# Kernel optimization log

Hardware: AMD Instinct MI355X
Metric: run time of the kernel (lower is better)

## Reference

```python
import jax, jax.numpy as jnp
import numpy as np

V, D, H, B, T = 50000, 256, 512, 64, 512
FORGET_BIAS = 1.0  # TF LSTMCell default

def setup_inputs() -> dict:
    key = jax.random.key(0)
    k1, k2, k3, k4 = jax.random.split(key, 4)
    word_indices = jax.random.randint(k1, (B, T), 0, V, dtype=jnp.int32)
    num_words = jax.random.randint(k2, (B,), 1, T + 1, dtype=jnp.int32)
    # Embedding: uniform(-1, 1) per original
    W_emb = jax.random.uniform(k3, (V, D), minval=-1.0, maxval=1.0, dtype=jnp.float32)
    # TF LSTMCell: single kernel [(D+H), 4H] with gate order i, j, f, o; zero bias
    kernel = jax.random.normal(k4, (D + H, 4 * H), dtype=jnp.float32) * 0.02
    bias = jnp.zeros((4 * H,), dtype=jnp.float32)
    return {"word_indices": word_indices, "num_words": num_words,
            "W_emb": W_emb, "kernel": kernel, "bias": bias}

def reference(word_indices, num_words, W_emb, kernel, bias):
    # embedding lookup: [B, T, D]
    x = W_emb[word_indices]
    xs = jnp.swapaxes(x, 0, 1)  # [T, B, D] time-major
    ts = jnp.arange(xs.shape[0])
    c0 = jnp.zeros((word_indices.shape[0], H), dtype=x.dtype)
    h0 = jnp.zeros_like(c0)

    def step(carry, inp):
        c, h = carry
        x_t, t = inp
        gates = jnp.concatenate([x_t, h], axis=-1) @ kernel + bias  # [B, 4H]
        i, j, f, o = jnp.split(gates, 4, axis=-1)
        c_new = jax.nn.sigmoid(f + FORGET_BIAS) * c + jax.nn.sigmoid(i) * jnp.tanh(j)
        h_new = jax.nn.sigmoid(o) * jnp.tanh(c_new)
        # static_rnn sequence_length semantics: copy state through past the end
        mask = (t < num_words)[:, None]
        c = jnp.where(mask, c_new, c)
        h = jnp.where(mask, h_new, h)
        return (c, h), None

    (c_fin, h_fin), _ = jax.lax.scan(step, (c0, h0), (xs, ts))
    # TF LSTM final_state = LSTMStateTuple(c, h); stack for a single array output
    return jnp.stack([c_fin, h_fin], axis=0)  # [2, B, H]
```

## Files before the change

kernel.cpp:

```cpp
#include <hip/hip_runtime.h>
#include <stdint.h>


#define NWG     64
#define NTHR    256
#define TSTEPS  512
#define BATCH   64
#define EDIM    256
#define HID     512
#define GCOLS   2048

typedef __attribute__((ext_vector_type(8))) short short8;
typedef __attribute__((ext_vector_type(4))) float f32x4;


__device__ __forceinline__ unsigned short f2bf(float f) {
  unsigned u = __float_as_uint(f);
  unsigned r = (u + 0x7FFFu + ((u >> 16) & 1u)) >> 16;
  return (unsigned short)r;
}
__device__ __forceinline__ float sigf(float x) {
  x = fminf(fmaxf(x, -30.0f), 30.0f);
  return 1.0f / (1.0f + __expf(-x));
}
__device__ __forceinline__ float tanh_fast(float x) {
  x = fminf(fmaxf(x, -15.0f), 15.0f);
  float e = __expf(-2.0f * x);
  return (1.0f - e) / (1.0f + e);
}
__device__ __forceinline__ void lstm_cell(float gi, float gj, float gf, float go,
                                          int t, int nw, float& c, float& h) {
  float cn = sigf(gf + 1.0f) * c + sigf(gi) * tanh_fast(gj);
  float hn = sigf(go) * tanh_fast(cn);
  if (t < nw) { c = cn; h = hn; }
}

__global__ void init_ws(unsigned* ws, int nwords) {
  int i = blockIdx.x * 256 + threadIdx.x;
  if (i < nwords) ws[i] = 0u;
}

__global__ void embed_k(const int* __restrict__ widx, const float* __restrict__ Wemb,
                        unsigned short* __restrict__ xb) {
  int tb = blockIdx.x;
  int t = tb >> 6, b = tb & 63;
  int wi = widx[b * TSTEPS + t];
  const float* src = Wemb + (size_t)wi * EDIM + threadIdx.x * 4;
  float4 v = *(const float4*)src;
  ushort4 o;
  o.x = f2bf(v.x); o.y = f2bf(v.y); o.z = f2bf(v.z); o.w = f2bf(v.w);
  *(ushort4*)(xb + (size_t)tb * EDIM + threadIdx.x * 4) = o;
}

__launch_bounds__(NTHR, 1)
__global__ void lstm_persist(const int* __restrict__ num_words,
                             const int* __restrict__ widx,
                             const float* __restrict__ Wemb,
                             const float* __restrict__ Wk,
                             const float* __restrict__ bias,
                             const unsigned short* __restrict__ xb,
                             unsigned short* __restrict__ hb0,
                             unsigned short* __restrict__ hb1,
                             unsigned* flags,
                             float* __restrict__ out,
                             int has_xb)
{
  __shared__ alignas(16) short Wlds[24576];
  __shared__ alignas(16) unsigned short hstg[1024];

  const int tid  = threadIdx.x;
  const int lane = tid & 63;
  const int wv   = tid >> 6;
  const int u0   = blockIdx.x * 8;

  for (int q = tid; q < 3072; q += NTHR) {
    int lq = q & 63;
    int kkn = q >> 6;
    int nt = (kkn >= 24) ? 1 : 0;
    int kk = kkn - nt * 24;
    int kbase = kk * 32 + ((lq >> 4) << 3);
    int nn = (nt << 4) + (lq & 15);
    int gcol = ((nn >> 3) << 9) + u0 + (nn & 7);
    short8 v;
#pragma unroll
    for (int j = 0; j < 8; ++j)
      v[j] = (short)f2bf(Wk[(size_t)(kbase + j) * GCOLS + gcol]);
    *(short8*)&Wlds[q * 8] = v;
  }

  const int n   = lane & 15;
  const int q4  = lane >> 4;
  const int bb  = wv * 16 + n;
  const int kq  = q4 << 3;
  const int un  = n & 7;
  const bool lo = (n < 8);

  float bias_g[4];
#pragma unroll
  for (int g = 0; g < 4; ++g) bias_g[g] = bias[g * HID + u0 + un];
  int nw_r[4];
#pragma unroll
  for (int r = 0; r < 4; ++r) nw_r[r] = num_words[wv * 16 + q4 * 4 + r];

  float c_r[4] = {0.f, 0.f, 0.f, 0.f};
  float h_r[4] = {0.f, 0.f, 0.f, 0.f};

  unsigned* myflag = flags + ((blockIdx.x << 2) + wv) * 32;
  const unsigned* fp = flags + ((lane << 2) + wv) * 32;

  unsigned short* hb[2] = {hb0, hb1};

  float4 pfw[16];
  uint4  pfx[8];
  auto PREFETCH = [&](int tt) {
    if (has_xb) {
      const unsigned short* xrow = xb + ((size_t)tt * BATCH + bb) * EDIM + kq;
#pragma unroll
      for (int kk = 0; kk < 8; ++kk)
        pfx[kk] = *(const uint4*)(xrow + kk * 32);
    } else {
      int wi = widx[bb * TSTEPS + tt];
      const float* er = Wemb + (size_t)wi * EDIM + kq;
#pragma unroll
      for (int kk = 0; kk < 8; ++kk) {
        pfw[2 * kk]     = *(const float4*)(er + kk * 32);
        pfw[2 * kk + 1] = *(const float4*)(er + kk * 32 + 4);
      }
    }
  };
  PREFETCH(0);

  __syncthreads();

  for (int t = 0; t < TSTEPS; ++t) {
    f32x4 acc0 = {0.f, 0.f, 0.f, 0.f};
    f32x4 acc1 = {0.f, 0.f, 0.f, 0.f};
    uint4 av[16];

    if (t > 0) {
      const unsigned tgt = (unsigned)t;
      for (;;) {
        unsigned v;
        asm volatile("global_load_dword %0, %1, off sc0 sc1\n\t"
                     "s_waitcnt vmcnt(0)" : "=v"(v) : "v"(fp));
        if (__ballot(v >= tgt) == ~0ull) break;
      }
      const unsigned short* hr = hb[t & 1] + bb * HID + kq;
#pragma unroll
      for (int kk = 0; kk < 16; ++kk)
        asm volatile("global_load_dwordx4 %0, %1, off sc0 sc1"
                     : "=v"(av[kk]) : "v"(hr + kk * 32));
    }

#pragma unroll
    for (int kk = 0; kk < 8; ++kk) {
      short8 a;
      if (has_xb) {
        a = __builtin_bit_cast(short8, pfx[kk]);
      } else {
        float4 f0 = pfw[2 * kk], f1 = pfw[2 * kk + 1];
        a[0] = (short)f2bf(f0.x); a[1] = (short)f2bf(f0.y);
        a[2] = (short)f2bf(f0.z); a[3] = (short)f2bf(f0.w);
        a[4] = (short)f2bf(f1.x); a[5] = (short)f2bf(f1.y);
        a[6] = (short)f2bf(f1.z); a[7] = (short)f2bf(f1.w);
      }
      short8 w0 = *(const short8*)&Wlds[((kk)      * 64 + lane) * 8];
      short8 w1 = *(const short8*)&Wlds[((24 + kk) * 64 + lane) * 8];
      acc0 = __builtin_amdgcn_mfma_f32_16x16x32_bf16(a, w0, acc0, 0, 0, 0);
      acc1 = __builtin_amdgcn_mfma_f32_16x16x32_bf16(a, w1, acc1, 0, 0, 0);
    }

    if (t > 0) {
      asm volatile("s_waitcnt vmcnt(0)" ::: "memory");
      __builtin_amdgcn_sched_barrier(0);
#pragma unroll
      for (int kk = 0; kk < 16; ++kk) {
        short8 a  = __builtin_bit_cast(short8, av[kk]);
        short8 w0 = *(const short8*)&Wlds[((8 + kk)  * 64 + lane) * 8];
        short8 w1 = *(const short8*)&Wlds[((32 + kk) * 64 + lane) * 8];
        acc0 = __builtin_amdgcn_mfma_f32_16x16x32_bf16(a, w0, acc0, 0, 0, 0);
        acc1 = __builtin_amdgcn_mfma_f32_16x16x32_bf16(a, w1, acc1, 0, 0, 0);
      }
    }

#pragma unroll
    for (int r = 0; r < 4; ++r) {
      float a0o = acc0[r], a1o = acc1[r];
      float a0x = __shfl_xor(a0o, 8);
      float a1x = __shfl_xor(a1o, 8);
      float gi = lo ? a0o : a0x;
      float gj = lo ? a0x : a0o;
      float gf = lo ? a1o : a1x;
      float go = lo ? a1x : a1o;
      lstm_cell(gi + bias_g[0], gj + bias_g[1], gf + bias_g[2], go + bias_g[3],
                t, nw_r[r], c_r[r], h_r[r]);
    }

    if (t + 1 < TSTEPS) {
      unsigned short* hw = hb[(t + 1) & 1];
      if (lo) {
#pragma unroll
        for (int r = 0; r < 4; ++r)
          hstg[wv * 256 + (q4 * 4 + r) * 8 + un] = f2bf(h_r[r]);
      }
      asm volatile("s_waitcnt lgkmcnt(0)" ::: "memory");
      {
        int row = lane >> 2, p = lane & 3;
        unsigned hv = *(const unsigned*)&hstg[wv * 256 + row * 8 + p * 2];
        unsigned* dst = (unsigned*)(hw + (size_t)(wv * 16 + row) * HID + u0) + p;
        asm volatile("global_store_dword %0, %1, off sc0 sc1"
                     :: "v"(dst), "v"(hv) : "memory");
      }
      PREFETCH(t + 1);
      if (has_xb)
        asm volatile("s_waitcnt vmcnt(8)" ::: "memory");
      else
        asm volatile("s_waitcnt vmcnt(16)" ::: "memory");
      if (lane == 0) {
        unsigned fv = (unsigned)(t + 1);
        asm volatile("global_store_dword %0, %1, off sc0 sc1"
                     :: "v"(myflag), "v"(fv) : "memory");
      }
    }
  }

  if (lo) {
#pragma unroll
    for (int r = 0; r < 4; ++r) {
      int b = wv * 16 + q4 * 4 + r;
      out[b * HID + u0 + un]                   = c_r[r];
      out[BATCH * HID + b * HID + u0 + un]     = h_r[r];
    }
  }
}

extern "C" void kernel_launch(void* const* d_in, const int* in_sizes, int n_in,
                              void* d_out, int out_size, void* d_ws, size_t ws_size,
                              hipStream_t stream) {
  const int*   widx = (const int*)d_in[0];
  const int*   nw   = (const int*)d_in[1];
  const float* Wemb = (const float*)d_in[2];
  const float* Wk   = (const float*)d_in[3];
  const float* bias = (const float*)d_in[4];
  float* out = (float*)d_out;
  char* ws = (char*)d_ws;

  unsigned* flags       = (unsigned*)(ws + 256);
  unsigned short* hb0   = (unsigned short*)(ws + 33280);
  unsigned short* hb1   = (unsigned short*)(ws + 98816);
  unsigned short* xb    = (unsigned short*)(ws + 164352);

  size_t need = 164352ull + (size_t)TSTEPS * BATCH * EDIM * 2;
  int has_xb = (ws_size >= need) ? 1 : 0;

  const int init_words = 164352 / 4;
  init_ws<<<(init_words + 255) / 256, 256, 0, stream>>>((unsigned*)ws, init_words);
  if (has_xb)
    embed_k<<<TSTEPS * BATCH, 64, 0, stream>>>(widx, Wemb, xb);

  void* args[] = {(void*)&nw, (void*)&widx, (void*)&Wemb, (void*)&Wk, (void*)&bias,
                  (void*)&xb, (void*)&hb0, (void*)&hb1, (void*)&flags,
                  (void*)&out, (void*)&has_xb};
  (void)hipLaunchCooperativeKernel((void*)lstm_persist, dim3(NWG), dim3(NTHR), args, 0, stream);
}
```

Measured before the change: 2.405 ms.

## Split batch into two half-groups and ping-pong them to hide cross-block sync latency

The 64-row batch is split into two independent 32-row halves (A and B). Each half keeps its own flags and its own state, and the step alternates between them, so one half's MFMA work overlaps the flag polling and h loads of the other half. The separate embedding pre-pass kernel is dropped. Embedding rows are instead gathered inline and prefetched one half-step ahead, which removes a launch and the staging buffer. Each wave now runs twice as many 16-row MFMA passes with half the rows used, so per-step MFMA work goes up. Spin loops gain a bounded retry count, and a non-cooperative fallback launch is added.

```diff
diff --git a/kernel.cpp b/kernel.cpp
--- a/kernel.cpp
+++ b/kernel.cpp
@@ -40,33 +40,19 @@
   if (i < nwords) ws[i] = 0u;
 }
 
-__global__ void embed_k(const int* __restrict__ widx, const float* __restrict__ Wemb,
-                        unsigned short* __restrict__ xb) {
-  int tb = blockIdx.x;
-  int t = tb >> 6, b = tb & 63;
-  int wi = widx[b * TSTEPS + t];
-  const float* src = Wemb + (size_t)wi * EDIM + threadIdx.x * 4;
-  float4 v = *(const float4*)src;
-  ushort4 o;
-  o.x = f2bf(v.x); o.y = f2bf(v.y); o.z = f2bf(v.z); o.w = f2bf(v.w);
-  *(ushort4*)(xb + (size_t)tb * EDIM + threadIdx.x * 4) = o;
-}
-
 __launch_bounds__(NTHR, 1)
 __global__ void lstm_persist(const int* __restrict__ num_words,
                              const int* __restrict__ widx,
                              const float* __restrict__ Wemb,
                              const float* __restrict__ Wk,
                              const float* __restrict__ bias,
-                             const unsigned short* __restrict__ xb,
                              unsigned short* __restrict__ hb0,
                              unsigned short* __restrict__ hb1,
                              unsigned* flags,
-                             float* __restrict__ out,
-                             int has_xb)
+                             float* __restrict__ out)
 {
   __shared__ alignas(16) short Wlds[24576];
-  __shared__ alignas(16) unsigned short hstg[1024];
+  __shared__ alignas(16) unsigned short hstg[256];
 
   const int tid  = threadIdx.x;
   const int lane = tid & 63;
@@ -90,146 +76,234 @@
 
   const int n   = lane & 15;
   const int q4  = lane >> 4;
-  const int bb  = wv * 16 + n;
   const int kq  = q4 << 3;
   const int un  = n & 7;
   const bool lo = (n < 8);
+  const int bbA = wv * 8 + (n & 7);
+  const int bbB = 32 + bbA;
 
   float bias_g[4];
 #pragma unroll
   for (int g = 0; g < 4; ++g) bias_g[g] = bias[g * HID + u0 + un];
-  int nw_r[4];
-#pragma unroll
-  for (int r = 0; r < 4; ++r) nw_r[r] = num_words[wv * 16 + q4 * 4 + r];
-
-  float c_r[4] = {0.f, 0.f, 0.f, 0.f};
-  float h_r[4] = {0.f, 0.f, 0.f, 0.f};
-
-  unsigned* myflag = flags + ((blockIdx.x << 2) + wv) * 32;
-  const unsigned* fp = flags + ((lane << 2) + wv) * 32;
+  int nwA[4], nwB[4];
+#pragma unroll
+  for (int r = 0; r < 4; ++r) {
+    int row = ((q4 << 2) + r) & 7;
+    nwA[r] = num_words[wv * 8 + row];
+    nwB[r] = num_words[32 + wv * 8 + row];
+  }
+
+  float cA[4] = {0,0,0,0}, hA[4] = {0,0,0,0};
+  float cB[4] = {0,0,0,0}, hB[4] = {0,0,0,0};
+
+  unsigned* myflagA = flags + ((blockIdx.x << 2) + wv) * 32;
+  unsigned* myflagB = myflagA + 16;
+  const unsigned* fpA = flags + ((lane << 2) + wv) * 32;
+  const unsigned* fpB = fpA + 16;
 
   unsigned short* hb[2] = {hb0, hb1};
 
   float4 pfw[16];
-  uint4  pfx[8];
-  auto PREFETCH = [&](int tt) {
-    if (has_xb) {
-      const unsigned short* xrow = xb + ((size_t)tt * BATCH + bb) * EDIM + kq;
-#pragma unroll
-      for (int kk = 0; kk < 8; ++kk)
-        pfx[kk] = *(const uint4*)(xrow + kk * 32);
-    } else {
-      int wi = widx[bb * TSTEPS + tt];
-      const float* er = Wemb + (size_t)wi * EDIM + kq;
-#pragma unroll
-      for (int kk = 0; kk < 8; ++kk) {
-        pfw[2 * kk]     = *(const float4*)(er + kk * 32);
-        pfw[2 * kk + 1] = *(const float4*)(er + kk * 32 + 4);
-      }
+  uint4  av[16];
+  int wiA, wiB;
+  {
+    int wi0 = widx[bbA * TSTEPS + 0];
+    const float* er = Wemb + (size_t)wi0 * EDIM + kq;
+#pragma unroll
+    for (int kk = 0; kk < 8; ++kk) {
+      pfw[2 * kk]     = *(const float4*)(er + kk * 32);
+      pfw[2 * kk + 1] = *(const float4*)(er + kk * 32 + 4);
     }
-  };
-  PREFETCH(0);
+    wiA = widx[bbA * TSTEPS + 1];
+    wiB = widx[bbB * TSTEPS + 0];
+  }
 
   __syncthreads();
+  asm volatile("s_waitcnt vmcnt(0)" ::: "memory");
+  __builtin_amdgcn_sched_barrier(0);
 
   for (int t = 0; t < TSTEPS; ++t) {
-    f32x4 acc0 = {0.f, 0.f, 0.f, 0.f};
-    f32x4 acc1 = {0.f, 0.f, 0.f, 0.f};
-    uint4 av[16];
-
-    if (t > 0) {
-      const unsigned tgt = (unsigned)t;
-      for (;;) {
-        unsigned v;
-        asm volatile("global_load_dword %0, %1, off sc0 sc1\n\t"
-                     "s_waitcnt vmcnt(0)" : "=v"(v) : "v"(fp));
-        if (__ballot(v >= tgt) == ~0ull) break;
-      }
-      const unsigned short* hr = hb[t & 1] + bb * HID + kq;
-#pragma unroll
-      for (int kk = 0; kk < 16; ++kk)
-        asm volatile("global_load_dwordx4 %0, %1, off sc0 sc1"
-                     : "=v"(av[kk]) : "v"(hr + kk * 32));
-    }
-
-#pragma unroll
-    for (int kk = 0; kk < 8; ++kk) {
-      short8 a;
-      if (has_xb) {
-        a = __builtin_bit_cast(short8, pfx[kk]);
-      } else {
-        float4 f0 = pfw[2 * kk], f1 = pfw[2 * kk + 1];
-        a[0] = (short)f2bf(f0.x); a[1] = (short)f2bf(f0.y);
-        a[2] = (short)f2bf(f0.z); a[3] = (short)f2bf(f0.w);
-        a[4] = (short)f2bf(f1.x); a[5] = (short)f2bf(f1.y);
-        a[6] = (short)f2bf(f1.z); a[7] = (short)f2bf(f1.w);
-      }
-      short8 w0 = *(const short8*)&Wlds[((kk)      * 64 + lane) * 8];
-      short8 w1 = *(const short8*)&Wlds[((24 + kk) * 64 + lane) * 8];
-      acc0 = __builtin_amdgcn_mfma_f32_16x16x32_bf16(a, w0, acc0, 0, 0, 0);
-      acc1 = __builtin_amdgcn_mfma_f32_16x16x32_bf16(a, w1, acc1, 0, 0, 0);
-    }
-
-    if (t > 0) {
+    {
       asm volatile("s_waitcnt vmcnt(0)" ::: "memory");
       __builtin_amdgcn_sched_barrier(0);
-#pragma unroll
-      for (int kk = 0; kk < 16; ++kk) {
-        short8 a  = __builtin_bit_cast(short8, av[kk]);
-        short8 w0 = *(const short8*)&Wlds[((8 + kk)  * 64 + lane) * 8];
-        short8 w1 = *(const short8*)&Wlds[((32 + kk) * 64 + lane) * 8];
-        acc0 = __builtin_amdgcn_mfma_f32_16x16x32_bf16(a, w0, acc0, 0, 0, 0);
-        acc1 = __builtin_amdgcn_mfma_f32_16x16x32_bf16(a, w1, acc1, 0, 0, 0);
+      f32x4 acc0 = {0,0,0,0}, acc1 = {0,0,0,0};
+#pragma unroll
+      for (int kk = 0; kk < 8; ++kk) {
+        float4 f0 = pfw[2 * kk], f1 = pfw[2 * kk + 1];
+        short8 a;
+        a[0]=(short)f2bf(f0.x); a[1]=(short)f2bf(f0.y);
+        a[2]=(short)f2bf(f0.z); a[3]=(short)f2bf(f0.w);
+        a[4]=(short)f2bf(f1.x); a[5]=(short)f2bf(f1.y);
+        a[6]=(short)f2bf(f1.z); a[7]=(short)f2bf(f1.w);
+        acc0 = __builtin_amdgcn_mfma_f32_16x16x32_bf16(a, *(const short8*)&Wlds[((kk)*64+lane)*8],      acc0, 0,0,0);
+        acc1 = __builtin_amdgcn_mfma_f32_16x16x32_bf16(a, *(const short8*)&Wlds[((24+kk)*64+lane)*8],   acc1, 0,0,0);
+      }
+      unsigned fv = 0xFFFFFFFFu;
+      if (t > 0)
+        asm volatile("global_load_dword %0, %1, off sc0 sc1" : "=v"(fv) : "v"(fpB));
+      if (t > 0) {
+#pragma unroll
+        for (int kk = 0; kk < 16; ++kk) {
+          short8 a = __builtin_bit_cast(short8, av[kk]);
+          acc0 = __builtin_amdgcn_mfma_f32_16x16x32_bf16(a, *(const short8*)&Wlds[((8+kk)*64+lane)*8],  acc0, 0,0,0);
+          acc1 = __builtin_amdgcn_mfma_f32_16x16x32_bf16(a, *(const short8*)&Wlds[((32+kk)*64+lane)*8], acc1, 0,0,0);
+        }
+      }
+#pragma unroll
+      for (int r = 0; r < 4; ++r) {
+        float a0o = acc0[r], a1o = acc1[r];
+        float a0x = __shfl_xor(a0o, 8), a1x = __shfl_xor(a1o, 8);
+        float gi = lo ? a0o : a0x, gj = lo ? a0x : a0o;
+        float gf = lo ? a1o : a1x, go = lo ? a1x : a1o;
+        lstm_cell(gi + bias_g[0], gj + bias_g[1], gf + bias_g[2], go + bias_g[3],
+                  t, nwA[r], cA[r], hA[r]);
+      }
+      if (lo && q4 < 2) {
+#pragma unroll
+        for (int r = 0; r < 4; ++r)
+          hstg[wv * 64 + ((q4 << 2) + r) * 8 + un] = f2bf(hA[r]);
+      }
+      asm volatile("s_waitcnt lgkmcnt(0)" ::: "memory");
+      if (t > 0) {
+        asm volatile("s_waitcnt vmcnt(0)" ::: "memory");
+        __builtin_amdgcn_sched_barrier(0);
+        const unsigned tgt = (unsigned)t;
+        int tries = 0;
+        while (__ballot(fv >= tgt) != ~0ull) {
+          if (++tries > (1 << 20)) break;
+          asm volatile("global_load_dword %0, %1, off sc0 sc1\n\t"
+                       "s_waitcnt vmcnt(0)" : "=v"(fv) : "v"(fpB));
+          __builtin_amdgcn_sched_barrier(0);
+        }
+      }
+      const bool dostore = (t + 1 < TSTEPS);
+      if (dostore && lane < 32) {
+        int row = lane >> 2, p = lane & 3;
+        unsigned hv = *(const unsigned*)&hstg[wv * 64 + row * 8 + p * 2];
+        unsigned* dst = (unsigned*)(hb[(t+1)&1] + (size_t)(wv*8+row)*HID + u0) + p;
+        asm volatile("global_store_dword %0, %1, off sc0 sc1" :: "v"(dst), "v"(hv) : "memory");
+      }
+      {
+        const float* er = Wemb + (size_t)wiB * EDIM + kq;
+#pragma unroll
+        for (int kk = 0; kk < 8; ++kk) {
+          asm volatile("global_load_dwordx4 %0, %1, off" : "=v"(pfw[2*kk])   : "v"(er + kk*32));
+          asm volatile("global_load_dwordx4 %0, %1, off" : "=v"(pfw[2*kk+1]) : "v"(er + kk*32 + 4));
+        }
+        if (t > 0) {
+          const unsigned short* hr = hb[t & 1] + (size_t)bbB * HID + kq;
+#pragma unroll
+          for (int kk = 0; kk < 16; ++kk)
+            asm volatile("global_load_dwordx4 %0, %1, off sc0 sc1" : "=v"(av[kk]) : "v"(hr + kk*32));
+        }
+        const int* wp = widx + bbB * TSTEPS + ((t+1 < TSTEPS) ? t+1 : TSTEPS-1);
+        asm volatile("global_load_dword %0, %1, off" : "=v"(wiB) : "v"(wp));
+      }
+      if (dostore) {
+        if (t > 0) asm volatile("s_waitcnt vmcnt(33)" ::: "memory");
+        else       asm volatile("s_waitcnt vmcnt(17)" ::: "memory");
+        if (lane == 0) {
+          unsigned fvw = (unsigned)(t + 1);
+          asm volatile("global_store_dword %0, %1, off sc0 sc1" :: "v"(myflagA), "v"(fvw) : "memory");
+        }
       }
     }
-
+    {
+      asm volatile("s_waitcnt vmcnt(0)" ::: "memory");
+      __builtin_amdgcn_sched_barrier(0);
+      f32x4 acc0 = {0,0,0,0}, acc1 = {0,0,0,0};
+#pragma unroll
+      for (int kk = 0; kk < 8; ++kk) {
+        float4 f0 = pfw[2 * kk], f1 = pfw[2 * kk + 1];
+        short8 a;
+        a[0]=(short)f2bf(f0.x); a[1]=(short)f2bf(f0.y);
+        a[2]=(short)f2bf(f0.z); a[3]=(short)f2bf(f0.w);
+        a[4]=(short)f2bf(f1.x); a[5]=(short)f2bf(f1.y);
+        a[6]=(short)f2bf(f1.z); a[7]=(short)f2bf(f1.w);
+        acc0 = __builtin_amdgcn_mfma_f32_16x16x32_bf16(a, *(const short8*)&Wlds[((kk)*64+lane)*8],      acc0, 0,0,0);
+        acc1 = __builtin_amdgcn_mfma_f32_16x16x32_bf16(a, *(const short8*)&Wlds[((24+kk)*64+lane)*8],   acc1, 0,0,0);
+      }
+      unsigned fv = 0xFFFFFFFFu;
+      const bool more = (t + 1 < TSTEPS);
+      if (more)
+        asm volatile("global_load_dword %0, %1, off sc0 sc1" : "=v"(fv) : "v"(fpA));
+      if (t > 0) {
+#pragma unroll
+        for (int kk = 0; kk < 16; ++kk) {
+          short8 a = __builtin_bit_cast(short8, av[kk]);
+          acc0 = __builtin_amdgcn_mfma_f32_16x16x32_bf16(a, *(const short8*)&Wlds[((8+kk)*64+lane)*8],  acc0, 0,0,0);
+          acc1 = __builtin_amdgcn_mfma_f32_16x16x32_bf16(a, *(const short8*)&Wlds[((32+kk)*64+lane)*8], acc1, 0,0,0);
+        }
+      }
+#pragma unroll
+      for (int r = 0; r < 4; ++r) {
+        float a0o = acc0[r], a1o = acc1[r];
+        float a0x = __shfl_xor(a0o, 8), a1x = __shfl_xor(a1o, 8);
+        float gi = lo ? a0o : a0x, gj = lo ? a0x : a0o;
+        float gf = lo ? a1o : a1x, go = lo ? a1x : a1o;
+        lstm_cell(gi + bias_g[0], gj + bias_g[1], gf + bias_g[2], go + bias_g[3],
+                  t, nwB[r], cB[r], hB[r]);
+      }
+      if (more) {
+        if (lo && q4 < 2) {
+#pragma unroll
+          for (int r = 0; r < 4; ++r)
+            hstg[wv * 64 + ((q4 << 2) + r) * 8 + un] = f2bf(hB[r]);
+        }
+        asm volatile("s_waitcnt lgkmcnt(0)" ::: "memory");
+        {
+          asm volatile("s_waitcnt vmcnt(0)" ::: "memory");
+          __builtin_amdgcn_sched_barrier(0);
+          const unsigned tgt = (unsigned)(t + 1);
+          int tries = 0;
+          while (__ballot(fv >= tgt) != ~0ull) {
+            if (++tries > (1 << 20)) break;
+            asm volatile("global_load_dword %0, %1, off sc0 sc1\n\t"
+                         "s_waitcnt vmcnt(0)" : "=v"(fv) : "v"(fpA));
+            __builtin_amdgcn_sched_barrier(0);
+          }
+        }
+        if (lane < 32) {
+          int row = lane >> 2, p = lane & 3;
+          unsigned hv = *(const unsigned*)&hstg[wv * 64 + row * 8 + p * 2];
+          unsigned* dst = (unsigned*)(hb[(t+1)&1] + (size_t)(32+wv*8+row)*HID + u0) + p;
+          asm volatile("global_store_dword %0, %1, off sc0 sc1" :: "v"(dst), "v"(hv) : "memory");
+        }
+        {
+          const float* er = Wemb + (size_t)wiA * EDIM + kq;
+#pragma unroll
+          for (int kk = 0; kk < 8; ++kk) {
+            asm volatile("global_load_dwordx4 %0, %1, off" : "=v"(pfw[2*kk])   : "v"(er + kk*32));
+            asm volatile("global_load_dwordx4 %0, %1, off" : "=v"(pfw[2*kk+1]) : "v"(er + kk*32 + 4));
+          }
+          const unsigned short* hr = hb[(t+1) & 1] + (size_t)bbA * HID + kq;
+#pragma unroll
+          for (int kk = 0; kk < 16; ++kk)
+            asm volatile("global_load_dwordx4 %0, %1, off sc0 sc1" : "=v"(av[kk]) : "v"(hr + kk*32));
+          const int* wp = widx + bbA * TSTEPS + ((t+2 < TSTEPS) ? t+2 : TSTEPS-1);
+          asm volatile("global_load_dword %0, %1, off" : "=v"(wiA) : "v"(wp));
+        }
+        asm volatile("s_waitcnt vmcnt(33)" ::: "memory");
+        if (lane == 0) {
+          unsigned fvw = (unsigned)(t + 1);
+          asm volatile("global_store_dword %0, %1, off sc0 sc1" :: "v"(myflagB), "v"(fvw) : "memory");
+        }
+      }
+    }
+  }
+
+  asm volatile("s_waitcnt vmcnt(0)" ::: "memory");
+  __builtin_amdgcn_sched_barrier(0);
+
+  if (lo && q4 < 2) {
 #pragma unroll
     for (int r = 0; r < 4; ++r) {
-      float a0o = acc0[r], a1o = acc1[r];
-      float a0x = __shfl_xor(a0o, 8);
-      float a1x = __shfl_xor(a1o, 8);
-      float gi = lo ? a0o : a0x;
-      float gj = lo ? a0x : a0o;
-      float gf = lo ? a1o : a1x;
-      float go = lo ? a1x : a1o;
-      lstm_cell(gi + bias_g[0], gj + bias_g[1], gf + bias_g[2], go + bias_g[3],
-                t, nw_r[r], c_r[r], h_r[r]);
-    }
-
-    if (t + 1 < TSTEPS) {
-      unsigned short* hw = hb[(t + 1) & 1];
-      if (lo) {
-#pragma unroll
-        for (int r = 0; r < 4; ++r)
-          hstg[wv * 256 + (q4 * 4 + r) * 8 + un] = f2bf(h_r[r]);
-      }
-      asm volatile("s_waitcnt lgkmcnt(0)" ::: "memory");
-      {
-        int row = lane >> 2, p = lane & 3;
-        unsigned hv = *(const unsigned*)&hstg[wv * 256 + row * 8 + p * 2];
-        unsigned* dst = (unsigned*)(hw + (size_t)(wv * 16 + row) * HID + u0) + p;
-        asm volatile("global_store_dword %0, %1, off sc0 sc1"
-                     :: "v"(dst), "v"(hv) : "memory");
-      }
-      PREFETCH(t + 1);
-      if (has_xb)
-        asm volatile("s_waitcnt vmcnt(8)" ::: "memory");
-      else
-        asm volatile("s_waitcnt vmcnt(16)" ::: "memory");
-      if (lane == 0) {
-        unsigned fv = (unsigned)(t + 1);
-        asm volatile("global_store_dword %0, %1, off sc0 sc1"
-                     :: "v"(myflag), "v"(fv) : "memory");
-      }
-    }
-  }
-
-  if (lo) {
-#pragma unroll
-    for (int r = 0; r < 4; ++r) {
-      int b = wv * 16 + q4 * 4 + r;
-      out[b * HID + u0 + un]                   = c_r[r];
-      out[BATCH * HID + b * HID + u0 + un]     = h_r[r];
+      int row = (q4 << 2) + r;
+      int bA = wv * 8 + row, bB = bA + 32;
+      out[bA * HID + u0 + un]               = cA[r];
+      out[BATCH * HID + bA * HID + u0 + un] = hA[r];
+      out[bB * HID + u0 + un]               = cB[r];
+      out[BATCH * HID + bB * HID + u0 + un] = hB[r];
     }
   }
 }
@@ -245,21 +319,19 @@
   float* out = (float*)d_out;
   char* ws = (char*)d_ws;
 
-  unsigned* flags       = (unsigned*)(ws + 256);
-  unsigned short* hb0   = (unsigned short*)(ws + 33280);
-  unsigned short* hb1   = (unsigned short*)(ws + 98816);
-  unsigned short* xb    = (unsigned short*)(ws + 164352);
-
-  size_t need = 164352ull + (size_t)TSTEPS * BATCH * EDIM * 2;
-  int has_xb = (ws_size >= need) ? 1 : 0;
+  unsigned* flags     = (unsigned*)(ws + 256);
+  unsigned short* hb0 = (unsigned short*)(ws + 33280);
+  unsigned short* hb1 = (unsigned short*)(ws + 98816);
 
   const int init_words = 164352 / 4;
   init_ws<<<(init_words + 255) / 256, 256, 0, stream>>>((unsigned*)ws, init_words);
-  if (has_xb)
-    embed_k<<<TSTEPS * BATCH, 64, 0, stream>>>(widx, Wemb, xb);
 
   void* args[] = {(void*)&nw, (void*)&widx, (void*)&Wemb, (void*)&Wk, (void*)&bias,
-                  (void*)&xb, (void*)&hb0, (void*)&hb1, (void*)&flags,
-                  (void*)&out, (void*)&has_xb};
-  (void)hipLaunchCooperativeKernel((void*)lstm_persist, dim3(NWG), dim3(NTHR), args, 0, stream);
-}
+                  (void*)&hb0, (void*)&hb1, (void*)&flags, (void*)&out};
+  hipError_t e = hipLaunchCooperativeKernel((void*)lstm_persist, dim3(NWG), dim3(NTHR),
+                                            args, 0, stream);
+  if (e != hipSuccess) {
+    lstm_persist<<<dim3(NWG), dim3(NTHR), 0, stream>>>(
+        nw, widx, Wemb, Wk, bias, hb0, hb1, flags, out);
+  }
+}
```

New measurement: 4.293 ms. 1.79x slower.
